# Kernel optimization log

Hardware: AMD Instinct MI355X
Metric: run time of the kernel (lower is better)

## Reference

```python
import jax, jax.numpy as jnp
import numpy as np

TOPK = 8

def setup_inputs() -> dict:
    key = jax.random.key(0)
    k1, k2, k3, k4, k5 = jax.random.split(key, 5)
    B, S, D, E = 8, 2048, 4096, 64
    scale = 1.0 / np.sqrt(D)
    x = jax.random.normal(k1, (B, S, D), dtype=jnp.float32)
    Wr = jax.random.uniform(k2, (D, E), dtype=jnp.float32, minval=-scale, maxval=scale)
    br = jax.random.uniform(k3, (E,), dtype=jnp.float32, minval=-scale, maxval=scale)
    Wn = jax.random.uniform(k4, (D, E), dtype=jnp.float32, minval=-scale, maxval=scale)
    bn = jax.random.uniform(k5, (E,), dtype=jnp.float32, minval=-scale, maxval=scale)
    return {"x": x, "Wr": Wr, "br": br, "Wn": Wn, "bn": bn}

def reference(x, Wr, br, Wn, bn):
    B, S, D = x.shape
    E = Wr.shape[1]
    logits = jnp.einsum('bsd,de->bse', x, Wr) + br          # [B,S,E]
    # NOTE: original module computes noisy_logits = logits + randn*noisy_vec but
    # then takes topk/softmax on the CLEAN logits, so the noise branch is dead code.
    noisy_vec = jnp.einsum('bsd,de->bse', x, Wn) + bn       # computed, unused (faithful)
    del noisy_vec
    topk_vals, topk_idx = jax.lax.top_k(logits, TOPK)       # [B,S,K]
    T = B * S
    flat_vals = topk_vals.reshape(T, TOPK)
    flat_idx = topk_idx.reshape(T, TOPK)
    sparse = jnp.full((T, E), -jnp.inf, dtype=logits.dtype)
    sparse = sparse.at[jnp.arange(T)[:, None], flat_idx].set(flat_vals)
    router_scores = jax.nn.softmax(sparse, axis=-1).reshape(B, S, E)
    return router_scores, topk_idx
```

## Files before the change

### kernel.cpp

```cpp
#include <hip/hip_runtime.h>
#include <math.h>

#define DDIM 4096
#define EDIM 64
#define NROWS 16384
#define MBLK 32
#define KT 64
#define NKT (DDIM / KT)
#define TOPK_K 8
#define DIGIT_BIAS 0x00808080

typedef int i32x4 __attribute__((ext_vector_type(4)));

__device__ __forceinline__ int digits_of(float f) {
  int v = __float2int_rn(f);
  return (v + DIGIT_BIAS) ^ DIGIT_BIAS;
}

__device__ __forceinline__ unsigned perm_b32(unsigned a, unsigned b, unsigned sel) {
#if __has_builtin(__builtin_amdgcn_perm)
  return __builtin_amdgcn_perm(a, b, sel);
#else
  union { unsigned u[2]; unsigned char c[8]; } s; s.u[0] = b; s.u[1] = a;
  unsigned r = 0;
  for (int i = 0; i < 4; ++i) r |= (unsigned)s.c[(sel >> (8*i)) & 7] << (8*i);
  return r;
#endif
}

__global__ __launch_bounds__(256) void wr_convert(const float* __restrict__ Wr,
                                                  char* __restrict__ wl8) {
  int t = blockIdx.x * 256 + threadIdx.x;
  int e = t & 63, k16 = t >> 6;
  int kt64 = k16 >> 2, kgg = k16 & 3, nf = e >> 4, col = e & 15;
  int D[16];
  #pragma unroll
  for (int j = 0; j < 16; ++j)
    D[j] = digits_of(Wr[(size_t)(k16 * 16 + j) * EDIM + e] * 68719476736.0f);
  #pragma unroll
  for (int pl = 0; pl < 4; ++pl) {
    unsigned wv[4];
    #pragma unroll
    for (int g = 0; g < 4; ++g)
      wv[g] = ((unsigned)((D[4*g+0] >> (8*pl)) & 255))
            | ((unsigned)((D[4*g+1] >> (8*pl)) & 255) << 8)
            | ((unsigned)((D[4*g+2] >> (8*pl)) & 255) << 16)
            | ((unsigned)((D[4*g+3] >> (8*pl)) & 255) << 24);
    i32x4 val = {(int)wv[0], (int)wv[1], (int)wv[2], (int)wv[3]};
    *(i32x4*)(wl8 + (size_t)pl * 262144 + (size_t)(kt64 * 4 + nf) * 1024
              + (size_t)(kgg * 16 + col) * 16) = val;
  }
}

__global__ __launch_bounds__(512, 4) void router_fused(
    const float* __restrict__ x, const char* __restrict__ wl8,
    const float* __restrict__ br,
    float* __restrict__ out_scores, float* __restrict__ out_idx) {
  __shared__ __align__(16) char smem[3][24576];

  const int tid  = threadIdx.x;
  const int lane = tid & 63;
  const int w    = tid >> 6;
  const int mw   = w >> 2;
  const int nw   = w & 3;
  const int kg   = lane >> 4;
  const int row0 = blockIdx.x * MBLK;
  const int row_l = mw * 16 + (lane & 15);
  const int srow = w * 4 + (lane >> 4);
  const float bias = br[nw * 16 + (lane & 15)];

  i32x4 acc[5] = {};

  auto stage = [&](int t, int b) {
    #pragma unroll
    for (int i = 0; i < 2; ++i) {
      int c = w * 2 + i;
      int plane = c >> 2, nf = c & 3;
      const char* src = wl8 + (size_t)plane * 262144 +
                        (size_t)(t * 4 + nf) * 1024 + (size_t)lane * 16;
      __builtin_amdgcn_global_load_lds(
          (const __attribute__((address_space(1))) unsigned int*)(const void*)src,
          (__attribute__((address_space(3))) unsigned int*)(void*)&smem[b][c * 1024],
          16, 0, 0);
    }
    {
      int cc = lane & 15;
      const float* src = x + (size_t)(row0 + srow) * DDIM + t * KT
                           + ((cc ^ (srow & 7)) << 2);
      __builtin_amdgcn_global_load_lds(
          (const __attribute__((address_space(1))) unsigned int*)(const void*)src,
          (__attribute__((address_space(3))) unsigned int*)(void*)
              &smem[b][16384 + w * 1024],
          16, 0, 0);
    }
  };

  auto compute = [&](int b) {
    const char* Wb = smem[b];
    const char* Xb = smem[b] + 16384;
    float4 xv[4];
    #pragma unroll
    for (int c = 0; c < 4; ++c) {
      int chunk = (kg * 4 + c) ^ (row_l & 7);
      xv[c] = *(const float4*)(Xb + row_l * 256 + chunk * 16);
    }
    i32x4 a0, a1, a2, a3;
    #pragma unroll
    for (int g = 0; g < 4; ++g) {
      float4 v = xv[g];
      unsigned f0 = (unsigned)digits_of(v.x * 33554432.0f);
      unsigned f1 = (unsigned)digits_of(v.y * 33554432.0f);
      unsigned f2 = (unsigned)digits_of(v.z * 33554432.0f);
      unsigned f3 = (unsigned)digits_of(v.w * 33554432.0f);
      unsigned zl01 = perm_b32(f1, f0, 0x05010400u);
      unsigned zh01 = perm_b32(f1, f0, 0x07030602u);
      unsigned zl23 = perm_b32(f3, f2, 0x05010400u);
      unsigned zh23 = perm_b32(f3, f2, 0x07030602u);
      a0[g] = (int)perm_b32(zl23, zl01, 0x05040100u);
      a1[g] = (int)perm_b32(zl23, zl01, 0x07060302u);
      a2[g] = (int)perm_b32(zh23, zh01, 0x05040100u);
      a3[g] = (int)perm_b32(zh23, zh01, 0x07060302u);
    }
    i32x4 b0 = *(const i32x4*)(Wb + (0 * 4 + nw) * 1024 + lane * 16);
    i32x4 b1 = *(const i32x4*)(Wb + (1 * 4 + nw) * 1024 + lane * 16);
    i32x4 b2 = *(const i32x4*)(Wb + (2 * 4 + nw) * 1024 + lane * 16);
    i32x4 b3 = *(const i32x4*)(Wb + (3 * 4 + nw) * 1024 + lane * 16);

    acc[0] = __builtin_amdgcn_mfma_i32_16x16x64_i8(a3, b3, acc[0], 0, 0, 0);
    acc[1] = __builtin_amdgcn_mfma_i32_16x16x64_i8(a3, b2, acc[1], 0, 0, 0);
    acc[1] = __builtin_amdgcn_mfma_i32_16x16x64_i8(a2, b3, acc[1], 0, 0, 0);
    acc[2] = __builtin_amdgcn_mfma_i32_16x16x64_i8(a3, b1, acc[2], 0, 0, 0);
    acc[2] = __builtin_amdgcn_mfma_i32_16x16x64_i8(a2, b2, acc[2], 0, 0, 0);
    acc[2] = __builtin_amdgcn_mfma_i32_16x16x64_i8(a1, b3, acc[2], 0, 0, 0);
    acc[3] = __builtin_amdgcn_mfma_i32_16x16x64_i8(a3, b0, acc[3], 0, 0, 0);
    acc[3] = __builtin_amdgcn_mfma_i32_16x16x64_i8(a2, b1, acc[3], 0, 0, 0);
    acc[3] = __builtin_amdgcn_mfma_i32_16x16x64_i8(a1, b2, acc[3], 0, 0, 0);
    acc[3] = __builtin_amdgcn_mfma_i32_16x16x64_i8(a0, b3, acc[3], 0, 0, 0);
    acc[4] = __builtin_amdgcn_mfma_i32_16x16x64_i8(a2, b0, acc[4], 0, 0, 0);
    acc[4] = __builtin_amdgcn_mfma_i32_16x16x64_i8(a1, b1, acc[4], 0, 0, 0);
    acc[4] = __builtin_amdgcn_mfma_i32_16x16x64_i8(a0, b2, acc[4], 0, 0, 0);
  };

  auto step = [&](int t, int b) {
    if (t <= NKT - 3)      asm volatile("s_waitcnt vmcnt(6)" ::: "memory");
    else if (t == NKT - 2) asm volatile("s_waitcnt vmcnt(3)" ::: "memory");
    else                   asm volatile("s_waitcnt vmcnt(0)" ::: "memory");
    __builtin_amdgcn_sched_barrier(0);
    __builtin_amdgcn_s_barrier();
    __builtin_amdgcn_sched_barrier(0);
    compute(b);
    asm volatile("s_waitcnt lgkmcnt(0)" ::: "memory");
    __builtin_amdgcn_sched_barrier(0);
    __builtin_amdgcn_s_barrier();
    if (t + 3 < NKT) stage(t + 3, b);
  };

  stage(0, 0); stage(1, 1); stage(2, 2);
  for (int t = 0; t < 63; t += 3) {
    step(t, 0); step(t + 1, 1); step(t + 2, 2);
  }
  step(63, 0);

  double* ls = (double*)smem;
  {
    int cc = nw * 16 + (lane & 15);
    #pragma unroll
    for (int j = 0; j < 4; ++j) {
      int r = mw * 16 + (lane >> 4) * 4 + j;
      double lg = (double)acc[0][j] * 0x1p-13 + (double)acc[1][j] * 0x1p-21
                + (double)acc[2][j] * 0x1p-29 + (double)acc[3][j] * 0x1p-37
                + (double)acc[4][j] * 0x1p-45 + (double)bias;
      ls[r * 64 + cc] = lg;
    }
  }
  __syncthreads();

  for (int rr = 0; rr < 4; ++rr) {
    int r = w * 4 + rr;
    double v0 = ls[r * 64 + lane];
    double cur = v0;
    bool sel  = false;
    int myidx = 0;
    double maxv = 0.0;
    #pragma unroll
    for (int k = 0; k < TOPK_K; ++k) {
      double bv = cur;
      int    bi = lane;
      #pragma unroll
      for (int off = 32; off; off >>= 1) {
        double ov = __shfl_xor(bv, off);
        int    oi = __shfl_xor(bi, off);
        if (ov > bv || (ov == bv && oi < bi)) { bv = ov; bi = oi; }
      }
      if (k == 0) maxv = bv;
      if (lane == k) myidx = bi;
      if (lane == bi) { cur = -__builtin_inf(); sel = true; }
    }
    float pv = sel ? expf((float)(v0 - maxv)) : 0.f;
    float ssum = pv;
    #pragma unroll
    for (int off = 32; off; off >>= 1) ssum += __shfl_xor(ssum, off);

    size_t rg = (size_t)row0 + r;
    out_scores[rg * 64 + lane] = pv / ssum;
    if (lane < TOPK_K) out_idx[rg * 8 + lane] = (float)myidx;
  }
}

extern "C" void kernel_launch(void* const* d_in, const int* in_sizes, int n_in,
                              void* d_out, int out_size, void* d_ws, size_t ws_size,
                              hipStream_t stream) {
  const float* x  = (const float*)d_in[0];
  const float* Wr = (const float*)d_in[1];
  const float* br = (const float*)d_in[2];

  char* wl8 = (char*)d_ws;
  float* out_scores = (float*)d_out;
  float* out_idx    = out_scores + (size_t)NROWS * EDIM;

  wr_convert<<<64, 256, 0, stream>>>(Wr, wl8);
  router_fused<<<NROWS / MBLK, 512, 0, stream>>>(x, wl8, br, out_scores, out_idx);
}
```

Baseline: 128.6 us.

## Software-pipeline int8 MFMA loop: prefetch next tile operands during current MFMAs

Restructures the main K loop so each step loads and converts the next tile's X and W operands from LDS while the current tile's MFMAs run, using double-buffered register operand sets, and drops the second barrier per step by issuing the global-to-LDS stage right after the first barrier. Address arithmetic is hoisted into precomputed base pointers. The X digit conversion switches from round-to-nearest to truncation, which is cheaper but changes the numerical result slightly. Register pressure rises from holding two operand sets, and reusing an LDS buffer with only one barrier per step depends on careful ordering.

```diff
diff --git a/kernel.cpp b/kernel.cpp
--- a/kernel.cpp
+++ b/kernel.cpp
@@ -6,14 +6,18 @@
 #define NROWS 16384
 #define MBLK 32
 #define KT 64
-#define NKT (DDIM / KT)
+#define NKT 64
 #define TOPK_K 8
 #define DIGIT_BIAS 0x00808080
 
 typedef int i32x4 __attribute__((ext_vector_type(4)));
 
-__device__ __forceinline__ int digits_of(float f) {
+__device__ __forceinline__ int digits_rn(float f) {
   int v = __float2int_rn(f);
+  return (v + DIGIT_BIAS) ^ DIGIT_BIAS;
+}
+__device__ __forceinline__ int digits_tz(float f) {
+  int v = (int)f;
   return (v + DIGIT_BIAS) ^ DIGIT_BIAS;
 }
 
@@ -36,7 +40,7 @@
   int D[16];
   #pragma unroll
   for (int j = 0; j < 16; ++j)
-    D[j] = digits_of(Wr[(size_t)(k16 * 16 + j) * EDIM + e] * 68719476736.0f);
+    D[j] = digits_rn(Wr[(size_t)(k16 * 16 + j) * EDIM + e] * 68719476736.0f);
   #pragma unroll
   for (int pl = 0; pl < 4; ++pl) {
     unsigned wv[4];
@@ -52,11 +56,28 @@
   }
 }
 
+#define STEP(T, SB, RB, AC, BC, AN, BN, VM, DOSTAGE) do {              \
+    asm volatile("s_waitcnt vmcnt(" #VM ")" ::: "memory");             \
+    __builtin_amdgcn_sched_barrier(0);                                 \
+    __builtin_amdgcn_s_barrier();                                      \
+    __builtin_amdgcn_sched_barrier(0);                                 \
+    if (DOSTAGE) stage((T) + 3, (SB));                                 \
+    float4 xv[4];                                                      \
+    ldX((RB), xv); ldB((RB), BN);                                      \
+    cvtg(xv[0], AN, 0); mf3a(AC, BC);                                  \
+    cvtg(xv[1], AN, 1); mf3b(AC, BC);                                  \
+    cvtg(xv[2], AN, 2); mf3c(AC, BC);                                  \
+    cvtg(xv[3], AN, 3); mf4d(AC, BC);                                  \
+    asm volatile("s_waitcnt lgkmcnt(0)" ::: "memory");                 \
+    __builtin_amdgcn_sched_barrier(0);                                 \
+  } while (0)
+
 __global__ __launch_bounds__(512, 4) void router_fused(
     const float* __restrict__ x, const char* __restrict__ wl8,
     const float* __restrict__ br,
     float* __restrict__ out_scores, float* __restrict__ out_idx) {
   __shared__ __align__(16) char smem[3][24576];
+  char* sb = (char*)smem;
 
   const int tid  = threadIdx.x;
   const int lane = tid & 63;
@@ -70,96 +91,105 @@
   const float bias = br[nw * 16 + (lane & 15)];
 
   i32x4 acc[5] = {};
-
+  i32x4 A0[4], A1[4], B0[4], B1[4];
+
+  const unsigned wrd = (unsigned)(nw * 1024 + lane * 16);
+  unsigned xrd[4];
+  #pragma unroll
+  for (int c = 0; c < 4; ++c)
+    xrd[c] = 16384u + (unsigned)(row_l * 256) +
+             (unsigned)((((kg * 4 + c) ^ (row_l & 7)) << 4));
+  const int c0 = w * 2, c1 = w * 2 + 1;
+  const char* wsrc0 = wl8 + (size_t)(c0 >> 2) * 262144 + (size_t)(c0 & 3) * 1024 + (size_t)lane * 16;
+  const char* wsrc1 = wl8 + (size_t)(c1 >> 2) * 262144 + (size_t)(c1 & 3) * 1024 + (size_t)lane * 16;
+  const char* xsrc  = (const char*)x + ((size_t)(row0 + srow)) * (DDIM * 4)
+                      + (size_t)((((unsigned)lane & 15) ^ (unsigned)(srow & 7)) << 4);
+  char* wdst0 = sb + c0 * 1024;
+  char* wdst1 = sb + c1 * 1024;
+  char* xdst  = sb + 16384 + w * 1024;
+
+  auto gll = [](const char* src, char* dst) {
+    __builtin_amdgcn_global_load_lds(
+        (const __attribute__((address_space(1))) unsigned int*)(const void*)src,
+        (__attribute__((address_space(3))) unsigned int*)(void*)dst, 16, 0, 0);
+  };
   auto stage = [&](int t, int b) {
-    #pragma unroll
-    for (int i = 0; i < 2; ++i) {
-      int c = w * 2 + i;
-      int plane = c >> 2, nf = c & 3;
-      const char* src = wl8 + (size_t)plane * 262144 +
-                        (size_t)(t * 4 + nf) * 1024 + (size_t)lane * 16;
-      __builtin_amdgcn_global_load_lds(
-          (const __attribute__((address_space(1))) unsigned int*)(const void*)src,
-          (__attribute__((address_space(3))) unsigned int*)(void*)&smem[b][c * 1024],
-          16, 0, 0);
-    }
-    {
-      int cc = lane & 15;
-      const float* src = x + (size_t)(row0 + srow) * DDIM + t * KT
-                           + ((cc ^ (srow & 7)) << 2);
-      __builtin_amdgcn_global_load_lds(
-          (const __attribute__((address_space(1))) unsigned int*)(const void*)src,
-          (__attribute__((address_space(3))) unsigned int*)(void*)
-              &smem[b][16384 + w * 1024],
-          16, 0, 0);
-    }
-  };
-
-  auto compute = [&](int b) {
-    const char* Wb = smem[b];
-    const char* Xb = smem[b] + 16384;
+    gll(wsrc0 + (size_t)t * 4096, wdst0 + b * 24576);
+    gll(wsrc1 + (size_t)t * 4096, wdst1 + b * 24576);
+    gll(xsrc  + (size_t)t * 256,  xdst  + b * 24576);
+  };
+  auto ldB = [&](int RB, i32x4 (&Bn)[4]) {
+    #pragma unroll
+    for (int p = 0; p < 4; ++p)
+      Bn[p] = *(const i32x4*)(sb + RB * 24576 + p * 4096 + wrd);
+  };
+  auto ldX = [&](int RB, float4 (&xv)[4]) {
+    #pragma unroll
+    for (int c = 0; c < 4; ++c)
+      xv[c] = *(const float4*)(sb + RB * 24576 + xrd[c]);
+  };
+  auto cvtg = [&](const float4& v, i32x4 (&An)[4], int g) {
+    unsigned f0 = (unsigned)digits_tz(v.x * 33554432.0f);
+    unsigned f1 = (unsigned)digits_tz(v.y * 33554432.0f);
+    unsigned f2 = (unsigned)digits_tz(v.z * 33554432.0f);
+    unsigned f3 = (unsigned)digits_tz(v.w * 33554432.0f);
+    unsigned zl01 = perm_b32(f1, f0, 0x05010400u);
+    unsigned zh01 = perm_b32(f1, f0, 0x07030602u);
+    unsigned zl23 = perm_b32(f3, f2, 0x05010400u);
+    unsigned zh23 = perm_b32(f3, f2, 0x07030602u);
+    An[0][g] = (int)perm_b32(zl23, zl01, 0x05040100u);
+    An[1][g] = (int)perm_b32(zl23, zl01, 0x07060302u);
+    An[2][g] = (int)perm_b32(zh23, zh01, 0x05040100u);
+    An[3][g] = (int)perm_b32(zh23, zh01, 0x07060302u);
+  };
+  auto mf3a = [&](i32x4 (&a)[4], i32x4 (&b)[4]) {
+    acc[0] = __builtin_amdgcn_mfma_i32_16x16x64_i8(a[3], b[3], acc[0], 0, 0, 0);
+    acc[1] = __builtin_amdgcn_mfma_i32_16x16x64_i8(a[3], b[2], acc[1], 0, 0, 0);
+    acc[2] = __builtin_amdgcn_mfma_i32_16x16x64_i8(a[3], b[1], acc[2], 0, 0, 0);
+  };
+  auto mf3b = [&](i32x4 (&a)[4], i32x4 (&b)[4]) {
+    acc[3] = __builtin_amdgcn_mfma_i32_16x16x64_i8(a[3], b[0], acc[3], 0, 0, 0);
+    acc[4] = __builtin_amdgcn_mfma_i32_16x16x64_i8(a[2], b[0], acc[4], 0, 0, 0);
+    acc[1] = __builtin_amdgcn_mfma_i32_16x16x64_i8(a[2], b[3], acc[1], 0, 0, 0);
+  };
+  auto mf3c = [&](i32x4 (&a)[4], i32x4 (&b)[4]) {
+    acc[2] = __builtin_amdgcn_mfma_i32_16x16x64_i8(a[2], b[2], acc[2], 0, 0, 0);
+    acc[3] = __builtin_amdgcn_mfma_i32_16x16x64_i8(a[2], b[1], acc[3], 0, 0, 0);
+    acc[4] = __builtin_amdgcn_mfma_i32_16x16x64_i8(a[1], b[1], acc[4], 0, 0, 0);
+  };
+  auto mf4d = [&](i32x4 (&a)[4], i32x4 (&b)[4]) {
+    acc[2] = __builtin_amdgcn_mfma_i32_16x16x64_i8(a[1], b[3], acc[2], 0, 0, 0);
+    acc[3] = __builtin_amdgcn_mfma_i32_16x16x64_i8(a[1], b[2], acc[3], 0, 0, 0);
+    acc[4] = __builtin_amdgcn_mfma_i32_16x16x64_i8(a[0], b[2], acc[4], 0, 0, 0);
+    acc[3] = __builtin_amdgcn_mfma_i32_16x16x64_i8(a[0], b[3], acc[3], 0, 0, 0);
+  };
+
+  stage(0, 0); stage(1, 1); stage(2, 2);
+  asm volatile("s_waitcnt vmcnt(6)" ::: "memory");
+  __builtin_amdgcn_sched_barrier(0);
+  __builtin_amdgcn_s_barrier();
+  __builtin_amdgcn_sched_barrier(0);
+  {
     float4 xv[4];
-    #pragma unroll
-    for (int c = 0; c < 4; ++c) {
-      int chunk = (kg * 4 + c) ^ (row_l & 7);
-      xv[c] = *(const float4*)(Xb + row_l * 256 + chunk * 16);
-    }
-    i32x4 a0, a1, a2, a3;
-    #pragma unroll
-    for (int g = 0; g < 4; ++g) {
-      float4 v = xv[g];
-      unsigned f0 = (unsigned)digits_of(v.x * 33554432.0f);
-      unsigned f1 = (unsigned)digits_of(v.y * 33554432.0f);
-      unsigned f2 = (unsigned)digits_of(v.z * 33554432.0f);
-      unsigned f3 = (unsigned)digits_of(v.w * 33554432.0f);
-      unsigned zl01 = perm_b32(f1, f0, 0x05010400u);
-      unsigned zh01 = perm_b32(f1, f0, 0x07030602u);
-      unsigned zl23 = perm_b32(f3, f2, 0x05010400u);
-      unsigned zh23 = perm_b32(f3, f2, 0x07030602u);
-      a0[g] = (int)perm_b32(zl23, zl01, 0x05040100u);
-      a1[g] = (int)perm_b32(zl23, zl01, 0x07060302u);
-      a2[g] = (int)perm_b32(zh23, zh01, 0x05040100u);
-      a3[g] = (int)perm_b32(zh23, zh01, 0x07060302u);
-    }
-    i32x4 b0 = *(const i32x4*)(Wb + (0 * 4 + nw) * 1024 + lane * 16);
-    i32x4 b1 = *(const i32x4*)(Wb + (1 * 4 + nw) * 1024 + lane * 16);
-    i32x4 b2 = *(const i32x4*)(Wb + (2 * 4 + nw) * 1024 + lane * 16);
-    i32x4 b3 = *(const i32x4*)(Wb + (3 * 4 + nw) * 1024 + lane * 16);
-
-    acc[0] = __builtin_amdgcn_mfma_i32_16x16x64_i8(a3, b3, acc[0], 0, 0, 0);
-    acc[1] = __builtin_amdgcn_mfma_i32_16x16x64_i8(a3, b2, acc[1], 0, 0, 0);
-    acc[1] = __builtin_amdgcn_mfma_i32_16x16x64_i8(a2, b3, acc[1], 0, 0, 0);
-    acc[2] = __builtin_amdgcn_mfma_i32_16x16x64_i8(a3, b1, acc[2], 0, 0, 0);
-    acc[2] = __builtin_amdgcn_mfma_i32_16x16x64_i8(a2, b2, acc[2], 0, 0, 0);
-    acc[2] = __builtin_amdgcn_mfma_i32_16x16x64_i8(a1, b3, acc[2], 0, 0, 0);
-    acc[3] = __builtin_amdgcn_mfma_i32_16x16x64_i8(a3, b0, acc[3], 0, 0, 0);
-    acc[3] = __builtin_amdgcn_mfma_i32_16x16x64_i8(a2, b1, acc[3], 0, 0, 0);
-    acc[3] = __builtin_amdgcn_mfma_i32_16x16x64_i8(a1, b2, acc[3], 0, 0, 0);
-    acc[3] = __builtin_amdgcn_mfma_i32_16x16x64_i8(a0, b3, acc[3], 0, 0, 0);
-    acc[4] = __builtin_amdgcn_mfma_i32_16x16x64_i8(a2, b0, acc[4], 0, 0, 0);
-    acc[4] = __builtin_amdgcn_mfma_i32_16x16x64_i8(a1, b1, acc[4], 0, 0, 0);
-    acc[4] = __builtin_amdgcn_mfma_i32_16x16x64_i8(a0, b2, acc[4], 0, 0, 0);
-  };
-
-  auto step = [&](int t, int b) {
-    if (t <= NKT - 3)      asm volatile("s_waitcnt vmcnt(6)" ::: "memory");
-    else if (t == NKT - 2) asm volatile("s_waitcnt vmcnt(3)" ::: "memory");
-    else                   asm volatile("s_waitcnt vmcnt(0)" ::: "memory");
-    __builtin_amdgcn_sched_barrier(0);
-    __builtin_amdgcn_s_barrier();
-    __builtin_amdgcn_sched_barrier(0);
-    compute(b);
-    asm volatile("s_waitcnt lgkmcnt(0)" ::: "memory");
-    __builtin_amdgcn_sched_barrier(0);
-    __builtin_amdgcn_s_barrier();
-    if (t + 3 < NKT) stage(t + 3, b);
-  };
-
-  stage(0, 0); stage(1, 1); stage(2, 2);
-  for (int t = 0; t < 63; t += 3) {
-    step(t, 0); step(t + 1, 1); step(t + 2, 2);
-  }
-  step(63, 0);
+    ldX(0, xv); ldB(0, B0);
+    cvtg(xv[0], A0, 0); cvtg(xv[1], A0, 1); cvtg(xv[2], A0, 2); cvtg(xv[3], A0, 3);
+  }
+  asm volatile("s_waitcnt lgkmcnt(0)" ::: "memory");
+  __builtin_amdgcn_sched_barrier(0);
+
+  for (int t = 0; t < 60; t += 6) {
+    STEP(t + 0, 0, 1, A0, B0, A1, B1, 3, 1);
+    STEP(t + 1, 1, 2, A1, B1, A0, B0, 3, 1);
+    STEP(t + 2, 2, 0, A0, B0, A1, B1, 3, 1);
+    STEP(t + 3, 0, 1, A1, B1, A0, B0, 3, 1);
+    STEP(t + 4, 1, 2, A0, B0, A1, B1, 3, 1);
+    STEP(t + 5, 2, 0, A1, B1, A0, B0, 3, 1);
+  }
+  STEP(60, 0, 1, A0, B0, A1, B1, 3, 1);
+  STEP(61, 1, 2, A1, B1, A0, B0, 3, 0);
+  STEP(62, 2, 0, A0, B0, A1, B1, 0, 0);
+  mf3a(A1, B1); mf3b(A1, B1); mf3c(A1, B1); mf4d(A1, B1);
+  __syncthreads();
 
   double* ls = (double*)smem;
   {
```

Measured after the change: 123.8 us. 1.04x faster.
